# Performance work log

Measured on AMD Instinct MI355X. Metric: run time of the kernel, lower is better.

Reference implementation:

```python
import jax, jax.numpy as jnp
import numpy as np

EPS = 1e-5

def _batchnorm(x, gamma, beta):
    # training-mode BatchNorm1d: biased variance over the batch axis
    mean = jnp.mean(x, axis=0)
    var = jnp.mean(jnp.square(x - mean), axis=0)
    return (x - mean) * jax.lax.rsqrt(var + EPS) * gamma + beta

def setup_inputs() -> dict:
    key = jax.random.key(0)
    ks = jax.random.split(key, 20)
    N, E, T = 100000, 400000, 1000000
    ATOM, BOND, ANGLE = 128, 128, 64
    s = 0.05
    return {
        "vertex_feat": jax.random.normal(ks[0], (N, ATOM), jnp.float32),
        "edge_feat": jax.random.normal(ks[1], (E, BOND), jnp.float32),
        "angle_feat": jax.random.normal(ks[2], (T, ANGLE), jnp.float32),
        "edge_index": jax.random.randint(ks[3], (2, E), 0, N),
        "k_idx": jax.random.randint(ks[4], (T,), 0, E),   # b_i: bond indices
        "j_idx": jax.random.randint(ks[5], (T,), 0, N),   # a: center atom indices
        "i_idx": jax.random.randint(ks[6], (T,), 0, N),   # b_j: indexes vertex rows per source code
        "w_core_src": jax.random.normal(ks[7], (BOND, ATOM), jnp.float32) * s,
        "w_core_dst": jax.random.normal(ks[8], (BOND, ATOM), jnp.float32) * s,
        "w_core_bond": jax.random.normal(ks[9], (BOND, BOND), jnp.float32) * s,
        "w_core_angle": jax.random.normal(ks[10], (BOND, ANGLE), jnp.float32) * s,
        "w_gate_src": jax.random.normal(ks[11], (BOND, ATOM), jnp.float32) * s,
        "w_gate_dst": jax.random.normal(ks[12], (BOND, ATOM), jnp.float32) * s,
        "w_gate_bond": jax.random.normal(ks[13], (BOND, BOND), jnp.float32) * s,
        "w_gate_angle": jax.random.normal(ks[14], (BOND, ANGLE), jnp.float32) * s,
        "bn_core_gamma": jnp.ones((BOND,), jnp.float32),
        "bn_core_beta": jnp.zeros((BOND,), jnp.float32),
        "bn_gate_gamma": jnp.ones((BOND,), jnp.float32),
        "bn_gate_beta": jnp.zeros((BOND,), jnp.float32),
        "w_out": jax.random.normal(ks[15], (BOND, BOND), jnp.float32) * s,
    }

def _branch(vertex_feat, edge_feat, angle_feat, k_idx, j_idx, i_idx, ws, wd, wb, wa):
    # reverse_scatter chain == gather-add:
    # out[t] = (angle @ wa.T)[t] + (v @ ws.T)[j_idx[t]] + (e @ wb.T)[k_idx[t]] + (v @ wd.T)[i_idx[t]]
    center = vertex_feat @ ws.T            # [N, bond]
    bond_i = edge_feat @ wb.T              # [E, bond]
    bond_j = vertex_feat @ wd.T            # [N, bond]
    angles = angle_feat @ wa.T             # [T, bond]
    return angles + center[j_idx] + bond_i[k_idx] + bond_j[i_idx]

def reference(vertex_feat, edge_feat, angle_feat, edge_index, k_idx, j_idx, i_idx,
              w_core_src, w_core_dst, w_core_bond, w_core_angle,
              w_gate_src, w_gate_dst, w_gate_bond, w_gate_angle,
              bn_core_gamma, bn_core_beta, bn_gate_gamma, bn_gate_beta, w_out):
    E = edge_feat.shape[0]
    core = _branch(vertex_feat, edge_feat, angle_feat, k_idx, j_idx, i_idx,
                   w_core_src, w_core_dst, w_core_bond, w_core_angle)   # [T, bond]
    gate = _branch(vertex_feat, edge_feat, angle_feat, k_idx, j_idx, i_idx,
                   w_gate_src, w_gate_dst, w_gate_bond, w_gate_angle)   # [T, bond]
    core = jax.nn.silu(_batchnorm(core, bn_core_gamma, bn_core_beta))
    gate = jax.nn.sigmoid(_batchnorm(gate, bn_gate_gamma, bn_gate_beta))
    update = core * gate                                                # [T, bond]
    new_bond = jax.ops.segment_sum(update, k_idx, num_segments=E)       # [E, bond]
    new_bond = new_bond @ w_out.T
    return new_bond + edge_feat
```

## Files before the change

### kernel.cpp

```cpp
#include <hip/hip_runtime.h>
#include <hip/hip_bf16.h>

typedef unsigned short u16;
typedef unsigned int u32;
typedef __attribute__((ext_vector_type(8))) short bf8;
typedef __attribute__((ext_vector_type(4))) float f32x4;

__device__ __forceinline__ float bf2f(u16 u) {
    u32 v = ((u32)u) << 16;
    float f;
    __builtin_memcpy(&f, &v, 4);
    return f;
}
__device__ __forceinline__ u16 f2bf(float f) {
    u32 v;
    __builtin_memcpy(&v, &f, 4);
    u32 r = (v + 0x7fffu + ((v >> 16) & 1u)) >> 16;
    return (u16)r;
}
__device__ __forceinline__ u32 pk2(float a, float b) {
    return (u32)f2bf(a) | ((u32)f2bf(b) << 16);
}
__device__ __forceinline__ void unpack4(uint2 u, float* f) {
    f[0] = bf2f((u16)(u.x & 0xffffu));
    f[1] = bf2f((u16)(u.x >> 16));
    f[2] = bf2f((u16)(u.y & 0xffffu));
    f[3] = bf2f((u16)(u.y >> 16));
}

#define BM 128
#define BN 128
#define BK 64
#define LSTR 72

__global__ void detect_dtype(const u16* __restrict__ v, int* __restrict__ flag)
{
    __shared__ int red[256];
    int tid = threadIdx.x;
    int cnt = 0;
    for (int i = tid; i < 8192; i += 256) {
        u16 u = v[2 * i];
        int e = (u >> 7) & 0xFF;
        cnt += (e >= 160) ? 1 : 0;
    }
    red[tid] = cnt;
    __syncthreads();
    for (int s = 128; s > 0; s >>= 1) {
        if (tid < s) red[tid] += red[tid + s];
        __syncthreads();
    }
    if (tid == 0) flag[0] = (red[0] > 400) ? 1 : 0;
}

__global__ __launch_bounds__(256)
void gemm_bt(const void* __restrict__ Av, const u16* __restrict__ W,
             u16* __restrict__ C, const int* __restrict__ flag,
             int M, int K, int Ncols)
{
    __shared__ u16 As[BM][LSTR];
    __shared__ u16 Ws[BN][LSTR];
    const bool isf32 = flag[0] != 0;
    const int tid = threadIdx.x;
    const int m0 = blockIdx.x * BM;
    const int n0 = blockIdx.y * BN;
    const int wave = tid >> 6, lane = tid & 63;
    const int l16 = lane & 15, quad = lane >> 4;
    const int wrow = (wave >> 1) * 64, wcol = (wave & 1) * 64;

    f32x4 acc[4][4];
    for (int mi = 0; mi < 4; ++mi)
        for (int ni = 0; ni < 4; ++ni)
            for (int r = 0; r < 4; ++r) acc[mi][ni][r] = 0.f;

    for (int kk = 0; kk < K; kk += BK) {
        for (int it = 0; it < 4; ++it) {
            int c = tid + it * 256;
            int row = c >> 3, col8 = (c & 7) * 8;
            uint4 v = make_uint4(0, 0, 0, 0);
            int gr = m0 + row;
            if (gr < M) {
                if (!isf32) {
                    v = *(const uint4*)((const u16*)Av + (size_t)gr * K + (kk + col8));
                } else {
                    const float* Af = (const float*)Av + (size_t)gr * K + (kk + col8);
                    float4 x = *(const float4*)Af;
                    float4 y = *(const float4*)(Af + 4);
                    v = make_uint4(pk2(x.x, x.y), pk2(x.z, x.w), pk2(y.x, y.y), pk2(y.z, y.w));
                }
            }
            *(uint4*)(&As[row][col8]) = v;
        }
        for (int it = 0; it < 4; ++it) {
            int c = tid + it * 256;
            int row = c >> 3, col8 = (c & 7) * 8;
            uint4 v = *(const uint4*)(W + (size_t)(n0 + row) * K + (kk + col8));
            *(uint4*)(&Ws[row][col8]) = v;
        }
        __syncthreads();
        for (int ko = 0; ko < BK; ko += 32) {
            bf8 af[4], bw[4];
            for (int mi = 0; mi < 4; ++mi)
                af[mi] = *(const bf8*)(&As[wrow + mi * 16 + l16][ko + quad * 8]);
            for (int ni = 0; ni < 4; ++ni)
                bw[ni] = *(const bf8*)(&Ws[wcol + ni * 16 + l16][ko + quad * 8]);
            for (int mi = 0; mi < 4; ++mi)
                for (int ni = 0; ni < 4; ++ni)
                    acc[mi][ni] = __builtin_amdgcn_mfma_f32_16x16x32_bf16(
                        af[mi], bw[ni], acc[mi][ni], 0, 0, 0);
        }
        __syncthreads();
    }
    for (int mi = 0; mi < 4; ++mi) {
        int rbase = m0 + wrow + mi * 16 + quad * 4;
        for (int r = 0; r < 4; ++r) {
            int row = rbase + r;
            if (row >= M) continue;
            for (int ni = 0; ni < 4; ++ni) {
                int col = n0 + wcol + ni * 16 + l16;
                C[(size_t)row * Ncols + col] = f2bf(acc[mi][ni][r]);
            }
        }
    }
}

__global__ __launch_bounds__(256)
void gemm_angle_fused(const void* __restrict__ Av, const u16* __restrict__ Wa,
                      const u16* __restrict__ Vout, const u16* __restrict__ Eout,
                      const int* __restrict__ jidx, const int* __restrict__ kidx,
                      const int* __restrict__ iidx,
                      u16* __restrict__ CG, float* __restrict__ stats2,
                      const int* __restrict__ flag, int T)
{
    __shared__ u16 sh[2 * BM * LSTR];
    u16 (*As)[LSTR] = (u16(*)[LSTR])sh;
    u16 (*Ws)[LSTR] = (u16(*)[LSTR])(sh + BM * LSTR);
    const bool isf32 = flag[0] != 0;
    const int tid = threadIdx.x;
    const int m0 = blockIdx.x * BM;
    const int h = blockIdx.y;
    const int n0 = h * 128;
    const int wave = tid >> 6, lane = tid & 63;
    const int l16 = lane & 15, quad = lane >> 4;
    const int wrow = (wave >> 1) * 64, wcol = (wave & 1) * 64;

    f32x4 acc[4][4];
    for (int mi = 0; mi < 4; ++mi)
        for (int ni = 0; ni < 4; ++ni)
            for (int r = 0; r < 4; ++r) acc[mi][ni][r] = 0.f;

    for (int it = 0; it < 4; ++it) {
        int c = tid + it * 256;
        int row = c >> 3, col8 = (c & 7) * 8;
        uint4 v = make_uint4(0, 0, 0, 0);
        int gr = m0 + row;
        if (gr < T) {
            if (!isf32) {
                v = *(const uint4*)((const u16*)Av + (size_t)gr * 64 + col8);
            } else {
                const float* Af = (const float*)Av + (size_t)gr * 64 + col8;
                float4 x = *(const float4*)Af;
                float4 y = *(const float4*)(Af + 4);
                v = make_uint4(pk2(x.x, x.y), pk2(x.z, x.w), pk2(y.x, y.y), pk2(y.z, y.w));
            }
        }
        *(uint4*)(&As[row][col8]) = v;
    }
    for (int it = 0; it < 4; ++it) {
        int c = tid + it * 256;
        int row = c >> 3, col8 = (c & 7) * 8;
        uint4 v = *(const uint4*)(Wa + (size_t)(n0 + row) * 64 + col8);
        *(uint4*)(&Ws[row][col8]) = v;
    }
    __syncthreads();
    for (int ko = 0; ko < 64; ko += 32) {
        bf8 af[4], bw[4];
        for (int mi = 0; mi < 4; ++mi)
            af[mi] = *(const bf8*)(&As[wrow + mi * 16 + l16][ko + quad * 8]);
        for (int ni = 0; ni < 4; ++ni)
            bw[ni] = *(const bf8*)(&Ws[wcol + ni * 16 + l16][ko + quad * 8]);
        for (int mi = 0; mi < 4; ++mi)
            for (int ni = 0; ni < 4; ++ni)
                acc[mi][ni] = __builtin_amdgcn_mfma_f32_16x16x32_bf16(
                    af[mi], bw[ni], acc[mi][ni], 0, 0, 0);
    }
    __syncthreads();

    u16 (*Cs)[136] = (u16(*)[136])sh;
    for (int mi = 0; mi < 4; ++mi) {
        int rbase = wrow + mi * 16 + quad * 4;
        for (int r = 0; r < 4; ++r)
            for (int ni = 0; ni < 4; ++ni)
                Cs[rbase + r][wcol + ni * 16 + l16] = f2bf(acc[mi][ni][r]);
    }
    __syncthreads();

    const int q = lane;
    const int p = q * 2;
    float sum0 = 0.f, sum1 = 0.f, ssq0 = 0.f, ssq1 = 0.f;
    for (int rr = wave; rr < 128; rr += 4) {
        long t = (long)m0 + rr;
        if (t >= T) break;
        int j = jidx[t], k = kidx[t], i = iidx[t];
        u32 ua = *(const u32*)(&Cs[rr][p]);
        u32 uj = *(const u32*)(Vout + (size_t)j * 512 + n0 + p);
        u32 uk = *(const u32*)(Eout + (size_t)k * 256 + n0 + p);
        u32 ui = *(const u32*)(Vout + (size_t)i * 512 + 256 + n0 + p);
        float v0 = bf2f((u16)(ua & 0xffffu)) + bf2f((u16)(uj & 0xffffu))
                 + bf2f((u16)(uk & 0xffffu)) + bf2f((u16)(ui & 0xffffu));
        float v1 = bf2f((u16)(ua >> 16)) + bf2f((u16)(uj >> 16))
                 + bf2f((u16)(uk >> 16)) + bf2f((u16)(ui >> 16));
        sum0 += v0; sum1 += v1;
        ssq0 += v0 * v0; ssq1 += v1 * v1;
        *(u32*)(CG + (size_t)t * 256 + n0 + p) = pk2(v0, v1);
    }

    __syncthreads();
    float* red = (float*)sh;
    red[wave * 128 + p] = sum0;
    red[wave * 128 + p + 1] = sum1;
    red[512 + wave * 128 + p] = ssq0;
    red[512 + wave * 128 + p + 1] = ssq1;
    __syncthreads();
    {
        int c = tid & 127, s = tid >> 7;
        float v = red[s * 512 + c] + red[s * 512 + 128 + c]
                + red[s * 512 + 256 + c] + red[s * 512 + 384 + c];
        atomicAdd(&stats2[(size_t)(blockIdx.x & 63) * 512 + s * 256 + n0 + c], v);
    }
}

__global__ __launch_bounds__(256)
void gemm_out(const float* __restrict__ Aacc, const void* __restrict__ Wv_,
              const void* __restrict__ Edgev, void* __restrict__ Outv,
              const int* __restrict__ flag, int M)
{
    __shared__ u16 As[BM][LSTR];
    __shared__ u16 Ws[BN][LSTR];
    const bool isf32 = flag[0] != 0;
    const int tid = threadIdx.x;
    const int m0 = blockIdx.x * BM;
    const int wave = tid >> 6, lane = tid & 63;
    const int l16 = lane & 15, quad = lane >> 4;
    const int wrow = (wave >> 1) * 64, wcol = (wave & 1) * 64;

    f32x4 acc[4][4];
    for (int mi = 0; mi < 4; ++mi)
        for (int ni = 0; ni < 4; ++ni)
            for (int r = 0; r < 4; ++r) acc[mi][ni][r] = 0.f;

    for (int kk = 0; kk < 128; kk += BK) {
        for (int it = 0; it < 4; ++it) {
            int c = tid + it * 256;
            int row = c >> 3, col8 = (c & 7) * 8;
            int gr = m0 + row;
            uint4 v = make_uint4(0, 0, 0, 0);
            if (gr < M) {
                const float* src = Aacc + (size_t)gr * 128 + kk + col8;
                v = make_uint4(pk2(src[0], src[1]), pk2(src[2], src[3]),
                               pk2(src[4], src[5]), pk2(src[6], src[7]));
            }
            *(uint4*)(&As[row][col8]) = v;
        }
        for (int it = 0; it < 4; ++it) {
            int c = tid + it * 256;
            int row = c >> 3, col8 = (c & 7) * 8;
            uint4 v;
            if (!isf32) {
                v = *(const uint4*)((const u16*)Wv_ + (size_t)row * 128 + (kk + col8));
            } else {
                const float* Wf = (const float*)Wv_ + (size_t)row * 128 + (kk + col8);
                float4 x = *(const float4*)Wf;
                float4 y = *(const float4*)(Wf + 4);
                v = make_uint4(pk2(x.x, x.y), pk2(x.z, x.w), pk2(y.x, y.y), pk2(y.z, y.w));
            }
            *(uint4*)(&Ws[row][col8]) = v;
        }
        __syncthreads();
        for (int ko = 0; ko < BK; ko += 32) {
            bf8 af[4], bw[4];
            for (int mi = 0; mi < 4; ++mi)
                af[mi] = *(const bf8*)(&As[wrow + mi * 16 + l16][ko + quad * 8]);
            for (int ni = 0; ni < 4; ++ni)
                bw[ni] = *(const bf8*)(&Ws[wcol + ni * 16 + l16][ko + quad * 8]);
            for (int mi = 0; mi < 4; ++mi)
                for (int ni = 0; ni < 4; ++ni)
                    acc[mi][ni] = __builtin_amdgcn_mfma_f32_16x16x32_bf16(
                        af[mi], bw[ni], acc[mi][ni], 0, 0, 0);
        }
        __syncthreads();
    }
    for (int mi = 0; mi < 4; ++mi) {
        int rbase = m0 + wrow + mi * 16 + quad * 4;
        for (int r = 0; r < 4; ++r) {
            int row = rbase + r;
            if (row >= M) continue;
            for (int ni = 0; ni < 4; ++ni) {
                int col = wcol + ni * 16 + l16;
                size_t idx = (size_t)row * 128 + col;
                float e = isf32 ? ((const float*)Edgev)[idx] : bf2f(((const u16*)Edgev)[idx]);
                float v = acc[mi][ni][r] + e;
                if (isf32) ((float*)Outv)[idx] = v;
                else       ((u16*)Outv)[idx] = f2bf(v);
            }
        }
    }
}

__global__ void bn_finalize(const float* __restrict__ stats2,
                            const void* __restrict__ gc, const void* __restrict__ bc,
                            const void* __restrict__ gg, const void* __restrict__ bg,
                            float* __restrict__ ab, const int* __restrict__ flag,
                            float invT)
{
    const bool isf32 = flag[0] != 0;
    int p = threadIdx.x;
    float s = 0.f, q = 0.f;
    for (int k = 0; k < 64; ++k) {
        s += stats2[(size_t)k * 512 + p];
        q += stats2[(size_t)k * 512 + 256 + p];
    }
    float mean = s * invT;
    float var = q * invT - mean * mean;
    const void* gsrc = (p < 128) ? gc : gg;
    const void* bsrc = (p < 128) ? bc : bg;
    int pi = p & 127;
    float g = isf32 ? ((const float*)gsrc)[pi] : bf2f(((const u16*)gsrc)[pi]);
    float b = isf32 ? ((const float*)bsrc)[pi] : bf2f(((const u16*)bsrc)[pi]);
    float a = g * rsqrtf(var + 1e-5f);
    ab[p] = a;
    ab[256 + p] = b - mean * a;
}


__global__ __launch_bounds__(256)
void hist_k(const int* __restrict__ kidx, int* __restrict__ cnt, int T)
{
    for (int t = blockIdx.x * 256 + threadIdx.x; t < T; t += gridDim.x * 256)
        atomicAdd(&cnt[kidx[t]], 1);
}

#define SCHUNK 2048

__global__ __launch_bounds__(256)
void scan_blocks(const int* __restrict__ cnt, int* __restrict__ bsum, int E)
{
    __shared__ int red[256];
    int b = blockIdx.x, t = threadIdx.x;
    int base = b * SCHUNK + t * 8;
    int s = 0;
    for (int i = 0; i < 8; ++i) {
        int idx = base + i;
        s += (idx < E) ? cnt[idx] : 0;
    }
    red[t] = s;
    __syncthreads();
    for (int st = 128; st > 0; st >>= 1) {
        if (t < st) red[t] += red[t + st];
        __syncthreads();
    }
    if (t == 0) bsum[b] = red[0];
}

__global__ void scan_partials(int* __restrict__ bsum, int NB,
                              int* __restrict__ offs, int E, int T)
{
    __shared__ int sh[256];
    int t = threadIdx.x;
    int v = (t < NB) ? bsum[t] : 0;
    sh[t] = v;
    __syncthreads();
    for (int d = 1; d < 256; d <<= 1) {
        int x = (t >= d) ? sh[t - d] : 0;
        __syncthreads();
        sh[t] += x;
        __syncthreads();
    }
    if (t < NB) bsum[t] = sh[t] - v;
    if (t == 0) offs[E] = T;
}

__global__ __launch_bounds__(256)
void scan_chunks(const int* __restrict__ cnt, const int* __restrict__ bsum,
                 int* __restrict__ offs, int E)
{
    __shared__ int sh[256];
    int b = blockIdx.x, t = threadIdx.x;
    int base = b * SCHUNK + t * 8;
    int loc[8];
    int s = 0;
    for (int i = 0; i < 8; ++i) {
        int idx = base + i;
        loc[i] = (idx < E) ? cnt[idx] : 0;
    }
    for (int i = 0; i < 8; ++i) { int v = loc[i]; loc[i] = s; s += v; }
    sh[t] = s;
    __syncthreads();
    for (int d = 1; d < 256; d <<= 1) {
        int x = (t >= d) ? sh[t - d] : 0;
        __syncthreads();
        sh[t] += x;
        __syncthreads();
    }
    int ex = sh[t] - s;
    int off = bsum[b] + ex;
    for (int i = 0; i < 8; ++i) {
        int idx = base + i;
        if (idx < E) offs[idx] = off + loc[i];
    }
}

__global__ __launch_bounds__(256)
void fill_k(const int* __restrict__ kidx, const int* __restrict__ offs,
            int* __restrict__ cur, int* __restrict__ blist, int T)
{
    for (int t = blockIdx.x * 256 + threadIdx.x; t < T; t += gridDim.x * 256) {
        int k = kidx[t];
        int pos = offs[k] + atomicAdd(&cur[k], 1);
        blist[pos] = t;
    }
}

__global__ __launch_bounds__(256)
void seg_update(const u16* __restrict__ CG, const float* __restrict__ ab,
                const int* __restrict__ offs, const int* __restrict__ blist,
                float* __restrict__ acc, int E)
{
    const int tid = threadIdx.x;
    const int q = tid & 63;
    const int wv = tid >> 6;
    const int f = q * 2;
    const float ac0 = ab[f], ac1 = ab[f + 1];
    const float ag0 = ab[128 + f], ag1 = ab[128 + f + 1];
    const float bc0 = ab[256 + f], bc1 = ab[256 + f + 1];
    const float bg0 = ab[384 + f], bg1 = ab[384 + f + 1];
    for (int e = blockIdx.x * 4 + wv; e < E; e += gridDim.x * 4) {
        int s = offs[e], en = offs[e + 1];
        float u0 = 0.f, u1 = 0.f;
        for (int idx = s; idx < en; ++idx) {
            int t = blist[idx];
            u32 c2 = *(const u32*)(CG + (size_t)t * 256 + f);
            u32 g2 = *(const u32*)(CG + (size_t)t * 256 + 128 + f);
            float c0 = bf2f((u16)(c2 & 0xffffu)) * ac0 + bc0;
            float c1 = bf2f((u16)(c2 >> 16)) * ac1 + bc1;
            float g0 = bf2f((u16)(g2 & 0xffffu)) * ag0 + bg0;
            float g1 = bf2f((u16)(g2 >> 16)) * ag1 + bg1;
            float s0 = 1.f / (1.f + __expf(-c0));
            float s1 = 1.f / (1.f + __expf(-c1));
            float t0 = 1.f / (1.f + __expf(-g0));
            float t1 = 1.f / (1.f + __expf(-g1));
            u0 += c0 * s0 * t0;
            u1 += c1 * s1 * t1;
        }
        *(float2*)(acc + (size_t)e * 128 + f) = make_float2(u0, u1);
    }
}

__device__ __forceinline__ u16 ld_bf(const void* p, size_t idx, bool isf32)
{
    return isf32 ? f2bf(((const float*)p)[idx]) : ((const u16*)p)[idx];
}

__global__ void pack_weights(const void* __restrict__ wcs, const void* __restrict__ wcd,
                             const void* __restrict__ wcb, const void* __restrict__ wca,
                             const void* __restrict__ wgs, const void* __restrict__ wgd,
                             const void* __restrict__ wgb, const void* __restrict__ wga,
                             u16* __restrict__ Wv, u16* __restrict__ We, u16* __restrict__ Wa,
                             const int* __restrict__ flag)
{
    const bool isf32 = flag[0] != 0;
    int tid = blockIdx.x * 256 + threadIdx.x;
    {
        int row = tid >> 7, col = tid & 127;
        const void* src = (row < 128) ? wcs : (row < 256) ? wgs : (row < 384) ? wcd : wgd;
        Wv[tid] = ld_bf(src, (size_t)(row & 127) * 128 + col, isf32);
    }
    if (tid < 256 * 128) {
        int row = tid >> 7, col = tid & 127;
        const void* src = (row < 128) ? wcb : wgb;
        We[tid] = ld_bf(src, (size_t)(row & 127) * 128 + col, isf32);
    }
    if (tid < 256 * 64) {
        int row = tid >> 6, col = tid & 63;
        const void* src = (row < 128) ? wca : wga;
        Wa[tid] = ld_bf(src, (size_t)(row & 127) * 64 + col, isf32);
    }
}

extern "C" void kernel_launch(void* const* d_in, const int* in_sizes, int n_in,
                              void* d_out, int out_size, void* d_ws, size_t ws_size,
                              hipStream_t stream)
{
    const void* vertex = d_in[0];
    const void* edge   = d_in[1];
    const void* angle  = d_in[2];
    const int* kidx = (const int*)d_in[4];
    const int* jidx = (const int*)d_in[5];
    const int* iidx = (const int*)d_in[6];

    const int N = in_sizes[0] / 128;
    const int E = in_sizes[1] / 128;
    const int T = in_sizes[2] / 64;

    char* p = (char*)d_ws;
    auto alloc = [&](size_t bytes) {
        char* r = p;
        p += (bytes + 255) & ~(size_t)255;
        return r;
    };
    u16* Wv = (u16*)alloc((size_t)512 * 128 * 2);
    u16* We = (u16*)alloc((size_t)256 * 128 * 2);
    u16* Wa = (u16*)alloc((size_t)256 * 64 * 2);
    float* stats2 = (float*)alloc((size_t)64 * 512 * 4);
    float* ab = (float*)alloc(512 * 4);
    int* flag = (int*)alloc(256);
    u16* Vout = (u16*)alloc((size_t)N * 512 * 2);
    u16* Eout = (u16*)alloc((size_t)E * 256 * 2);
    u16* CG   = (u16*)alloc((size_t)T * 256 * 2);
    float* acc = (float*)Vout;

    char* tail = (char*)acc + (size_t)E * 512;
    int* cnt   = (int*)tail;
    int* offs  = cnt + ((E + 63) & ~63);
    int* blist = offs + ((E + 1 + 63) & ~63);
    int* bsum  = blist + ((T + 63) & ~63);
    const int NB = (E + SCHUNK - 1) / SCHUNK;

    hipMemsetAsync(stats2, 0, (size_t)64 * 512 * 4, stream);
    detect_dtype<<<1, 256, 0, stream>>>((const u16*)vertex, flag);
    pack_weights<<<256, 256, 0, stream>>>(d_in[7], d_in[8], d_in[9], d_in[10],
                                          d_in[11], d_in[12], d_in[13], d_in[14],
                                          Wv, We, Wa, flag);
    gemm_bt<<<dim3((N + 127) / 128, 4), 256, 0, stream>>>(vertex, Wv, Vout, flag, N, 128, 512);
    gemm_bt<<<dim3((E + 127) / 128, 2), 256, 0, stream>>>(edge, We, Eout, flag, E, 128, 256);
    gemm_angle_fused<<<dim3((T + 127) / 128, 2), 256, 0, stream>>>(
        angle, Wa, Vout, Eout, jidx, kidx, iidx, CG, stats2, flag, T);

    hipMemsetAsync(cnt, 0, (size_t)E * 4, stream);
    hist_k<<<2048, 256, 0, stream>>>(kidx, cnt, T);
    scan_blocks<<<NB, 256, 0, stream>>>(cnt, bsum, E);
    scan_partials<<<1, 256, 0, stream>>>(bsum, NB, offs, E, T);
    scan_chunks<<<NB, 256, 0, stream>>>(cnt, bsum, offs, E);
    hipMemsetAsync(cnt, 0, (size_t)E * 4, stream);
    fill_k<<<2048, 256, 0, stream>>>(kidx, offs, cnt, blist, T);

    bn_finalize<<<1, 256, 0, stream>>>(stats2, d_in[15], d_in[16], d_in[17], d_in[18],
                                       ab, flag, 1.0f / (float)T);
    seg_update<<<2048, 256, 0, stream>>>(CG, ab, offs, blist, acc, E);
    gemm_out<<<dim3((E + 127) / 128, 1), 256, 0, stream>>>(acc, d_in[19], edge, d_out, flag, E);
}
```

Baseline: 1.909 ms.

## Shrink angle GEMM tile to 64 rows, read weights directly, swap grid axes

The fused angle GEMM now uses 64-row tiles with each wave owning a 32-column strip. Weight fragments are loaded straight from global memory instead of being staged in LDS, which cuts shared memory use to one buffer reused for the output tile and doubles the block count. Grid axes are swapped for the GEMMs so blocks that share the same A rows (the column halves or quarters) are scheduled next to each other, which should improve L2 reuse of the input rows. The cost is more redundant global weight reads per block and twice as many atomic stat reductions.

```diff
diff --git a/kernel.cpp b/kernel.cpp
--- a/kernel.cpp
+++ b/kernel.cpp
@@ -20,12 +20,6 @@
 }
 __device__ __forceinline__ u32 pk2(float a, float b) {
     return (u32)f2bf(a) | ((u32)f2bf(b) << 16);
-}
-__device__ __forceinline__ void unpack4(uint2 u, float* f) {
-    f[0] = bf2f((u16)(u.x & 0xffffu));
-    f[1] = bf2f((u16)(u.x >> 16));
-    f[2] = bf2f((u16)(u.y & 0xffffu));
-    f[3] = bf2f((u16)(u.y >> 16));
 }
 
 #define BM 128
@@ -61,8 +55,8 @@
     __shared__ u16 Ws[BN][LSTR];
     const bool isf32 = flag[0] != 0;
     const int tid = threadIdx.x;
-    const int m0 = blockIdx.x * BM;
-    const int n0 = blockIdx.y * BN;
+    const int m0 = blockIdx.y * BM;
+    const int n0 = blockIdx.x * BN;
     const int wave = tid >> 6, lane = tid & 63;
     const int l16 = lane & 15, quad = lane >> 4;
     const int wrow = (wave >> 1) * 64, wcol = (wave & 1) * 64;
@@ -131,24 +125,19 @@
                       u16* __restrict__ CG, float* __restrict__ stats2,
                       const int* __restrict__ flag, int T)
 {
-    __shared__ u16 sh[2 * BM * LSTR];
-    u16 (*As)[LSTR] = (u16(*)[LSTR])sh;
-    u16 (*Ws)[LSTR] = (u16(*)[LSTR])(sh + BM * LSTR);
+    __shared__ u16 sh[64 * 136];
+    u16 (*As)[72] = (u16(*)[72])sh;
+    u16 (*Cs)[136] = (u16(*)[136])sh;
     const bool isf32 = flag[0] != 0;
     const int tid = threadIdx.x;
-    const int m0 = blockIdx.x * BM;
-    const int h = blockIdx.y;
+    const int h = blockIdx.x;
     const int n0 = h * 128;
+    const int m0 = blockIdx.y * 64;
     const int wave = tid >> 6, lane = tid & 63;
     const int l16 = lane & 15, quad = lane >> 4;
-    const int wrow = (wave >> 1) * 64, wcol = (wave & 1) * 64;
-
-    f32x4 acc[4][4];
-    for (int mi = 0; mi < 4; ++mi)
-        for (int ni = 0; ni < 4; ++ni)
-            for (int r = 0; r < 4; ++r) acc[mi][ni][r] = 0.f;
-
-    for (int it = 0; it < 4; ++it) {
+    const int wcol = wave * 32;
+
+    for (int it = 0; it < 2; ++it) {
         int c = tid + it * 256;
         int row = c >> 3, col8 = (c & 7) * 8;
         uint4 v = make_uint4(0, 0, 0, 0);
@@ -165,46 +154,44 @@
         }
         *(uint4*)(&As[row][col8]) = v;
     }
-    for (int it = 0; it < 4; ++it) {
-        int c = tid + it * 256;
-        int row = c >> 3, col8 = (c & 7) * 8;
-        uint4 v = *(const uint4*)(Wa + (size_t)(n0 + row) * 64 + col8);
-        *(uint4*)(&Ws[row][col8]) = v;
-    }
-    __syncthreads();
+    __syncthreads();
+
+    f32x4 acc[4][2];
+    for (int mi = 0; mi < 4; ++mi)
+        for (int ni = 0; ni < 2; ++ni)
+            for (int r = 0; r < 4; ++r) acc[mi][ni][r] = 0.f;
+
     for (int ko = 0; ko < 64; ko += 32) {
-        bf8 af[4], bw[4];
+        bf8 af[4], bw[2];
         for (int mi = 0; mi < 4; ++mi)
-            af[mi] = *(const bf8*)(&As[wrow + mi * 16 + l16][ko + quad * 8]);
-        for (int ni = 0; ni < 4; ++ni)
-            bw[ni] = *(const bf8*)(&Ws[wcol + ni * 16 + l16][ko + quad * 8]);
+            af[mi] = *(const bf8*)(&As[mi * 16 + l16][ko + quad * 8]);
+        for (int ni = 0; ni < 2; ++ni)
+            bw[ni] = *(const bf8*)(Wa + (size_t)(n0 + wcol + ni * 16 + l16) * 64
+                                       + ko + quad * 8);
         for (int mi = 0; mi < 4; ++mi)
-            for (int ni = 0; ni < 4; ++ni)
+            for (int ni = 0; ni < 2; ++ni)
                 acc[mi][ni] = __builtin_amdgcn_mfma_f32_16x16x32_bf16(
                     af[mi], bw[ni], acc[mi][ni], 0, 0, 0);
     }
     __syncthreads();
 
-    u16 (*Cs)[136] = (u16(*)[136])sh;
-    for (int mi = 0; mi < 4; ++mi) {
-        int rbase = wrow + mi * 16 + quad * 4;
+    for (int mi = 0; mi < 4; ++mi)
         for (int r = 0; r < 4; ++r)
-            for (int ni = 0; ni < 4; ++ni)
-                Cs[rbase + r][wcol + ni * 16 + l16] = f2bf(acc[mi][ni][r]);
-    }
-    __syncthreads();
-
-    const int q = lane;
-    const int p = q * 2;
+            for (int ni = 0; ni < 2; ++ni)
+                Cs[mi * 16 + quad * 4 + r][wcol + ni * 16 + l16] = f2bf(acc[mi][ni][r]);
+    __syncthreads();
+
+    const int p = lane * 2;
     float sum0 = 0.f, sum1 = 0.f, ssq0 = 0.f, ssq1 = 0.f;
-    for (int rr = wave; rr < 128; rr += 4) {
-        long t = (long)m0 + rr;
+    for (int i = 0; i < 16; ++i) {
+        int rl = wave + 4 * i;
+        long t = (long)m0 + rl;
         if (t >= T) break;
-        int j = jidx[t], k = kidx[t], i = iidx[t];
-        u32 ua = *(const u32*)(&Cs[rr][p]);
+        int j = jidx[t], k = kidx[t], ii = iidx[t];
+        u32 ua = *(const u32*)(&Cs[rl][p]);
         u32 uj = *(const u32*)(Vout + (size_t)j * 512 + n0 + p);
         u32 uk = *(const u32*)(Eout + (size_t)k * 256 + n0 + p);
-        u32 ui = *(const u32*)(Vout + (size_t)i * 512 + 256 + n0 + p);
+        u32 ui = *(const u32*)(Vout + (size_t)ii * 512 + 256 + n0 + p);
         float v0 = bf2f((u16)(ua & 0xffffu)) + bf2f((u16)(uj & 0xffffu))
                  + bf2f((u16)(uk & 0xffffu)) + bf2f((u16)(ui & 0xffffu));
         float v1 = bf2f((u16)(ua >> 16)) + bf2f((u16)(uj >> 16))
@@ -225,7 +212,7 @@
         int c = tid & 127, s = tid >> 7;
         float v = red[s * 512 + c] + red[s * 512 + 128 + c]
                 + red[s * 512 + 256 + c] + red[s * 512 + 384 + c];
-        atomicAdd(&stats2[(size_t)(blockIdx.x & 63) * 512 + s * 256 + n0 + c], v);
+        atomicAdd(&stats2[(size_t)(blockIdx.y & 63) * 512 + s * 256 + n0 + c], v);
     }
 }
 
@@ -530,9 +517,9 @@
     pack_weights<<<256, 256, 0, stream>>>(d_in[7], d_in[8], d_in[9], d_in[10],
                                           d_in[11], d_in[12], d_in[13], d_in[14],
                                           Wv, We, Wa, flag);
-    gemm_bt<<<dim3((N + 127) / 128, 4), 256, 0, stream>>>(vertex, Wv, Vout, flag, N, 128, 512);
-    gemm_bt<<<dim3((E + 127) / 128, 2), 256, 0, stream>>>(edge, We, Eout, flag, E, 128, 256);
-    gemm_angle_fused<<<dim3((T + 127) / 128, 2), 256, 0, stream>>>(
+    gemm_bt<<<dim3(4, (N + 127) / 128), 256, 0, stream>>>(vertex, Wv, Vout, flag, N, 128, 512);
+    gemm_bt<<<dim3(2, (E + 127) / 128), 256, 0, stream>>>(edge, We, Eout, flag, E, 128, 256);
+    gemm_angle_fused<<<dim3(2, (T + 63) / 64), 256, 0, stream>>>(
         angle, Wa, Vout, Eout, jidx, kidx, iidx, CG, stats2, flag, T);
 
     hipMemsetAsync(cnt, 0, (size_t)E * 4, stream);
```

Result: slower. 1.958 ms (+2.6%).
